# Kernel tuning notes

Measured on AMD Instinct MI355X. Metric: run time of the kernel, lower is better.

Reference implementation:

```python
import jax, jax.numpy as jnp
import numpy as np

N = 2048

def setup_inputs() -> dict:
    key = jax.random.key(0)
    ks = jax.random.split(key, 7)
    x = jax.random.uniform(ks[0], (N,), dtype=jnp.float32) * 100.0  # time vector
    W1 = jax.random.normal(ks[1], (128, 2), dtype=jnp.float32) * 0.5
    b1 = jax.random.normal(ks[2], (128,), dtype=jnp.float32) * 0.1
    W2 = jax.random.normal(ks[3], (32, 128), dtype=jnp.float32) * 0.1
    b2 = jax.random.normal(ks[4], (32,), dtype=jnp.float32) * 0.1
    W3 = jax.random.normal(ks[5], (1, 32), dtype=jnp.float32) * 0.1
    b3 = jax.random.normal(ks[6], (1,), dtype=jnp.float32) * 0.1
    return {"x": x, "W1": W1, "b1": b1, "W2": W2, "b2": b2, "W3": W3, "b3": b3}

def reference(x, W1, b1, W2, b2, W3, b3):
    # Vectorized equivalent of the nested-loop pair build:
    # pairs (x[i], x[j]) for all j >= i (upper triangle incl. diagonal).
    n = x.shape[0]
    iu_r, iu_c = np.triu_indices(n)  # static index arrays, P = n(n+1)/2
    pairs = jnp.stack([x[iu_r], x[iu_c]], axis=-1)  # [P, 2]
    h = jax.nn.sigmoid(pairs @ W1.T + b1)           # [P, 128]
    h = jax.nn.relu(h @ W2.T + b2)                  # [P, 32]
    v = (h @ W3.T + b3)[:, 0]                       # [P]
    # K starts as eye; the loops overwrite the full upper triangle (incl. diag),
    # leaving the strictly-lower triangle at 0.
    K = jnp.zeros((n, n), dtype=x.dtype).at[iu_r, iu_c].set(v)
    return K.T @ K  # torch casts to double; kept float32 (jax x64 disabled)
```

## Files before the change

kernel.cpp:

```cpp
#include <hip/hip_runtime.h>
#include <hip/hip_bf16.h>

#define N 2048

using f32x4  = __attribute__((ext_vector_type(4))) float;
using short8 = __attribute__((ext_vector_type(8))) short;
using uint4v = __attribute__((ext_vector_type(4))) unsigned int;

#define GLOAD_LDS16(dst, src)                                                        \
  __builtin_amdgcn_global_load_lds((const __attribute__((address_space(1))) void*)(src), \
                                   (__attribute__((address_space(3))) void*)(dst), 16, 0, 0)

__global__ void prep(const float* __restrict__ W2, const float* __restrict__ W1,
                     const float* __restrict__ b1,
                     __hip_bfloat16* __restrict__ W2b,
                     float* __restrict__ W1n, float* __restrict__ b1n) {
  const float c = -1.4426950408889634f;
  int t = blockIdx.x * 256 + threadIdx.x;
  W2b[t] = __float2bfloat16(W2[t]);
  if (t < 256) W1n[t] = W1[t] * c;
  if (t < 128) b1n[t] = b1[t] * c;
}

__global__ void zero_A(uint4v* __restrict__ A4) {
  A4[blockIdx.x * 256 + threadIdx.x] = (uint4v){0u, 0u, 0u, 0u};
}

__global__ __launch_bounds__(256) void build_A_mfma(
    const float* __restrict__ x,
    const float* __restrict__ W1n,
    const float* __restrict__ b1n,
    const __hip_bfloat16* __restrict__ W2b,
    const float* __restrict__ b2,
    const float* __restrict__ W3,
    const float* __restrict__ b3,
    __hip_bfloat16* __restrict__ A)
{
  const int t = blockIdx.x;
  int bj = (int)((sqrtf(8.0f * (float)t + 1.0f) - 1.0f) * 0.5f);
  while ((bj + 1) * (bj + 2) / 2 <= t) ++bj;
  while (bj * (bj + 1) / 2 > t) --bj;
  const int bi = t - bj * (bj + 1) / 2;

  const int i0 = bi * 16, j0 = bj * 16;
  const int tid = threadIdx.x;

  __shared__ float w1s[256];
  __shared__ float b1s[128];
  w1s[tid] = W1n[tid & 255];
  if (tid < 128) b1s[tid] = b1n[tid];
  __syncthreads();

  const int w  = tid >> 6;
  const int l  = tid & 63;
  const int lm = l & 15;
  const int lk = l >> 4;

  const float xi = x[i0 + lm];
  float xj[4];
#pragma unroll
  for (int m = 0; m < 4; ++m) xj[m] = x[j0 + w * 4 + m];

  short8 wf[2][4];
#pragma unroll
  for (int g = 0; g < 2; ++g)
#pragma unroll
    for (int kb = 0; kb < 4; ++kb)
      wf[g][kb] = *(const short8*)(W2b + (g * 16 + lm) * 128 + kb * 32 + lk * 8);

  const float b2v[2] = {b2[lm], b2[16 + lm]};
  f32x4 acc[4][2];
#pragma unroll
  for (int m = 0; m < 4; ++m)
#pragma unroll
    for (int g = 0; g < 2; ++g)
      acc[m][g] = (f32x4){b2v[g], b2v[g], b2v[g], b2v[g]};

#pragma unroll
  for (int kb = 0; kb < 4; ++kb) {
    float base[8], w1b_[8];
#pragma unroll
    for (int e = 0; e < 8; ++e) {
      const int k = kb * 32 + lk * 8 + e;
      base[e]  = fmaf(w1s[2 * k], xi, b1s[k]);
      w1b_[e]  = w1s[2 * k + 1];
    }
#pragma unroll
    for (int m = 0; m < 4; ++m) {
      uint4v pk;
#pragma unroll
      for (int e2 = 0; e2 < 4; ++e2) {
        const float t0 = fmaf(w1b_[2 * e2],     xj[m], base[2 * e2]);
        const float t1 = fmaf(w1b_[2 * e2 + 1], xj[m], base[2 * e2 + 1]);
        const float h0 = __builtin_amdgcn_rcpf(1.0f + __builtin_amdgcn_exp2f(t0));
        const float h1 = __builtin_amdgcn_rcpf(1.0f + __builtin_amdgcn_exp2f(t1));
        const unsigned u0 = __builtin_bit_cast(unsigned, h0) + 0x8000u;
        const unsigned u1 = __builtin_bit_cast(unsigned, h1) + 0x8000u;
        pk[e2] = __builtin_amdgcn_perm(u1, u0, 0x07060302u);
      }
      const short8 af = __builtin_bit_cast(short8, pk);
      acc[m][0] = __builtin_amdgcn_mfma_f32_16x16x32_bf16(af, wf[0][kb], acc[m][0], 0, 0, 0);
      acc[m][1] = __builtin_amdgcn_mfma_f32_16x16x32_bf16(af, wf[1][kb], acc[m][1], 0, 0, 0);
    }
  }

  const float w3a = W3[lm], w3b = W3[16 + lm];
  const float b3v = b3[0];
  const int   rsel = l & 3;

#pragma unroll
  for (int m = 0; m < 4; ++m) {
    const int j = j0 + w * 4 + m;
    float v[4];
#pragma unroll
    for (int r = 0; r < 4; ++r) {
      float s = fmaf(fmaxf(acc[m][0][r], 0.0f), w3a,
                     fmaxf(acc[m][1][r], 0.0f) * w3b);
      s += __shfl_xor(s, 1);
      s += __shfl_xor(s, 2);
      s += __shfl_xor(s, 4);
      s += __shfl_xor(s, 8);
      v[r] = s + b3v;
    }
    const float sv = rsel == 0 ? v[0] : rsel == 1 ? v[1] : rsel == 2 ? v[2] : v[3];
    const int i = i0 + lk * 4 + rsel;
    if (lm < 4 && i <= j)
      A[(size_t)j * N + i] = __float2bfloat16(sv);
  }
}

__global__ __launch_bounds__(256) void gemm_ata(
    const __hip_bfloat16* __restrict__ A, float* __restrict__ C)
{
  __shared__ __align__(16) __hip_bfloat16 As[64 * 32];
  __shared__ __align__(16) __hip_bfloat16 Bs[64 * 32];

  const int m0 = blockIdx.y * 64;
  const int n0 = blockIdx.x * 64;
  const int tid = threadIdx.x;
  const int w  = tid >> 6;
  const int l  = tid & 63;
  const int wr = (w >> 1) * 32;
  const int wc = (w & 1) * 32;
  const int lm = l & 15;
  const int lk = l >> 4;

  f32x4 acc[2][2];
#pragma unroll
  for (int m = 0; m < 2; ++m)
#pragma unroll
    for (int n = 0; n < 2; ++n)
      acc[m][n] = (f32x4){0.f, 0.f, 0.f, 0.f};

  const int mn = m0 < n0 ? m0 : n0;
  const int ktiles = (mn + 64) >> 5;

  const int srow = 16 * w + (l >> 2);
  const int scol = (l & 3) * 8;

  for (int kt = 0; kt < ktiles; ++kt) {
    const int k0 = kt * 32;
    __syncthreads();
    GLOAD_LDS16(As + 16 * w * 32, A + (size_t)(m0 + srow) * N + k0 + scol);
    GLOAD_LDS16(Bs + 16 * w * 32, A + (size_t)(n0 + srow) * N + k0 + scol);
    __syncthreads();

    short8 af[2], bfr[2];
#pragma unroll
    for (int m = 0; m < 2; ++m)
      af[m] = *(const short8*)(As + (wr + m * 16 + lm) * 32 + lk * 8);
#pragma unroll
    for (int n = 0; n < 2; ++n)
      bfr[n] = *(const short8*)(Bs + (wc + n * 16 + lm) * 32 + lk * 8);

#pragma unroll
    for (int m = 0; m < 2; ++m)
#pragma unroll
      for (int n = 0; n < 2; ++n)
        acc[m][n] = __builtin_amdgcn_mfma_f32_16x16x32_bf16(af[m], bfr[n], acc[m][n], 0, 0, 0);
  }

#pragma unroll
  for (int m = 0; m < 2; ++m) {
    const int row = m0 + wr + m * 16 + lk * 4;
#pragma unroll
    for (int n = 0; n < 2; ++n) {
      const int col = n0 + wc + n * 16 + lm;
#pragma unroll
      for (int r = 0; r < 4; ++r)
        C[(size_t)(row + r) * N + col] = acc[m][n][r];
    }
  }
}

extern "C" void kernel_launch(void* const* d_in, const int* in_sizes, int n_in,
                              void* d_out, int out_size, void* d_ws, size_t ws_size,
                              hipStream_t stream) {
  const float* x  = (const float*)d_in[0];
  const float* W1 = (const float*)d_in[1];
  const float* b1 = (const float*)d_in[2];
  const float* W2 = (const float*)d_in[3];
  const float* b2 = (const float*)d_in[4];
  const float* W3 = (const float*)d_in[5];
  const float* b3 = (const float*)d_in[6];
  float* C = (float*)d_out;

  __hip_bfloat16* W2b = (__hip_bfloat16*)d_ws;
  float* W1n = (float*)((char*)d_ws + 8192);
  float* b1n = (float*)((char*)d_ws + 12288);
  __hip_bfloat16* A = (__hip_bfloat16*)((char*)d_ws + 16384);

  prep<<<dim3(16), dim3(256), 0, stream>>>(W2, W1, b1, W2b, W1n, b1n);
  zero_A<<<dim3(2048), dim3(256), 0, stream>>>((uint4v*)A);
  build_A_mfma<<<dim3(8256), dim3(256), 0, stream>>>(x, W1n, b1n, W2b, b2, W3, b3, A);
  gemm_ata<<<dim3(32, 32), dim3(256), 0, stream>>>(A, C);
}
```

Before: 179.0 us.

## Fuse prep with zeroing, pack sigmoid math, enlarge and double-buffer GEMM tiles

Merges the weight-prep and A-zeroing kernels into one launch. Rewrites the first-layer pre-activation as two-wide float vectors so the compiler can emit packed FMA and add. Changes the A^T A GEMM from 64x64 to 128x128 block tiles with a 4x4 MFMA accumulator grid per wave and double-buffered LDS staging to overlap loads with compute. The larger tiles cut redundant global reads but launch only 256 blocks, and the triangular k-range gives those blocks uneven work.

```diff
diff --git a/kernel.cpp b/kernel.cpp
--- a/kernel.cpp
+++ b/kernel.cpp
@@ -3,6 +3,7 @@
 
 #define N 2048
 
+using f32x2  = __attribute__((ext_vector_type(2))) float;
 using f32x4  = __attribute__((ext_vector_type(4))) float;
 using short8 = __attribute__((ext_vector_type(8))) short;
 using uint4v = __attribute__((ext_vector_type(4))) unsigned int;
@@ -11,19 +12,17 @@
   __builtin_amdgcn_global_load_lds((const __attribute__((address_space(1))) void*)(src), \
                                    (__attribute__((address_space(3))) void*)(dst), 16, 0, 0)
 
-__global__ void prep(const float* __restrict__ W2, const float* __restrict__ W1,
-                     const float* __restrict__ b1,
-                     __hip_bfloat16* __restrict__ W2b,
-                     float* __restrict__ W1n, float* __restrict__ b1n) {
+__global__ void prep_zero(const float* __restrict__ W2, const float* __restrict__ W1,
+                          const float* __restrict__ b1,
+                          __hip_bfloat16* __restrict__ W2b,
+                          float* __restrict__ W1n, float* __restrict__ b1n,
+                          uint4v* __restrict__ A4) {
+  const int t = blockIdx.x * 256 + threadIdx.x;
+  A4[t] = (uint4v){0u, 0u, 0u, 0u};
   const float c = -1.4426950408889634f;
-  int t = blockIdx.x * 256 + threadIdx.x;
-  W2b[t] = __float2bfloat16(W2[t]);
-  if (t < 256) W1n[t] = W1[t] * c;
-  if (t < 128) b1n[t] = b1[t] * c;
-}
-
-__global__ void zero_A(uint4v* __restrict__ A4) {
-  A4[blockIdx.x * 256 + threadIdx.x] = (uint4v){0u, 0u, 0u, 0u};
+  if (t < 4096) W2b[t] = __float2bfloat16(W2[t]);
+  if (t < 256)  W1n[t] = W1[t] * c;
+  if (t < 128)  b1n[t] = b1[t] * c;
 }
 
 __global__ __launch_bounds__(256) void build_A_mfma(
@@ -78,22 +77,27 @@
 
 #pragma unroll
   for (int kb = 0; kb < 4; ++kb) {
-    float base[8], w1b_[8];
-#pragma unroll
-    for (int e = 0; e < 8; ++e) {
-      const int k = kb * 32 + lk * 8 + e;
-      base[e]  = fmaf(w1s[2 * k], xi, b1s[k]);
-      w1b_[e]  = w1s[2 * k + 1];
+    f32x2 basep[4], w1bp[4];
+#pragma unroll
+    for (int e2 = 0; e2 < 4; ++e2) {
+      const int k = kb * 32 + lk * 8 + e2 * 2;
+      basep[e2] = (f32x2){fmaf(w1s[2 * k],     xi, b1s[k]),
+                          fmaf(w1s[2 * k + 2], xi, b1s[k + 1])};
+      w1bp[e2]  = (f32x2){w1s[2 * k + 1], w1s[2 * k + 3]};
     }
 #pragma unroll
     for (int m = 0; m < 4; ++m) {
+      const f32x2 xj2 = (f32x2){xj[m], xj[m]};
       uint4v pk;
 #pragma unroll
       for (int e2 = 0; e2 < 4; ++e2) {
-        const float t0 = fmaf(w1b_[2 * e2],     xj[m], base[2 * e2]);
-        const float t1 = fmaf(w1b_[2 * e2 + 1], xj[m], base[2 * e2 + 1]);
-        const float h0 = __builtin_amdgcn_rcpf(1.0f + __builtin_amdgcn_exp2f(t0));
-        const float h1 = __builtin_amdgcn_rcpf(1.0f + __builtin_amdgcn_exp2f(t1));
+        const f32x2 t01 = __builtin_elementwise_fma(w1bp[e2], xj2, basep[e2]);
+        f32x2 e01;
+        e01[0] = __builtin_amdgcn_exp2f(t01[0]);
+        e01[1] = __builtin_amdgcn_exp2f(t01[1]);
+        const f32x2 d01 = e01 + (f32x2){1.0f, 1.0f};
+        const float h0 = __builtin_amdgcn_rcpf(d01[0]);
+        const float h1 = __builtin_amdgcn_rcpf(d01[1]);
         const unsigned u0 = __builtin_bit_cast(unsigned, h0) + 0x8000u;
         const unsigned u1 = __builtin_bit_cast(unsigned, h1) + 0x8000u;
         pk[e2] = __builtin_amdgcn_perm(u1, u0, 0x07060302u);
@@ -132,59 +136,74 @@
 __global__ __launch_bounds__(256) void gemm_ata(
     const __hip_bfloat16* __restrict__ A, float* __restrict__ C)
 {
-  __shared__ __align__(16) __hip_bfloat16 As[64 * 32];
-  __shared__ __align__(16) __hip_bfloat16 Bs[64 * 32];
-
-  const int m0 = blockIdx.y * 64;
-  const int n0 = blockIdx.x * 64;
+  __shared__ __align__(16) __hip_bfloat16 As[2][128 * 32];
+  __shared__ __align__(16) __hip_bfloat16 Bs[2][128 * 32];
+
+  const int m0 = blockIdx.y * 128;
+  const int n0 = blockIdx.x * 128;
   const int tid = threadIdx.x;
   const int w  = tid >> 6;
   const int l  = tid & 63;
-  const int wr = (w >> 1) * 32;
-  const int wc = (w & 1) * 32;
+  const int wr = (w >> 1) * 64;
+  const int wc = (w & 1) * 64;
   const int lm = l & 15;
   const int lk = l >> 4;
 
-  f32x4 acc[2][2];
-#pragma unroll
-  for (int m = 0; m < 2; ++m)
-#pragma unroll
-    for (int n = 0; n < 2; ++n)
+  f32x4 acc[4][4];
+#pragma unroll
+  for (int m = 0; m < 4; ++m)
+#pragma unroll
+    for (int n = 0; n < 4; ++n)
       acc[m][n] = (f32x4){0.f, 0.f, 0.f, 0.f};
 
   const int mn = m0 < n0 ? m0 : n0;
-  const int ktiles = (mn + 64) >> 5;
-
-  const int srow = 16 * w + (l >> 2);
+  const int ktiles = (mn + 128) >> 5;
+
+  const int srow = l >> 2;
   const int scol = (l & 3) * 8;
 
+#define STAGE(kt, b)                                                                   \
+  {                                                                                    \
+    const int k0_ = (kt) * 32;                                                         \
+    _Pragma("unroll")                                                                  \
+    for (int c = 0; c < 2; ++c) {                                                      \
+      const int r0 = (w * 2 + c) * 16;                                                 \
+      GLOAD_LDS16(&As[b][r0 * 32], A + (size_t)(m0 + r0 + srow) * N + k0_ + scol);     \
+      GLOAD_LDS16(&Bs[b][r0 * 32], A + (size_t)(n0 + r0 + srow) * N + k0_ + scol);     \
+    }                                                                                  \
+  }
+
+  STAGE(0, 0);
+  __syncthreads();
+
   for (int kt = 0; kt < ktiles; ++kt) {
-    const int k0 = kt * 32;
+    const int cur = kt & 1;
+    if (kt + 1 < ktiles)
+      STAGE(kt + 1, cur ^ 1);
+
+    short8 af[4], bfr[4];
+#pragma unroll
+    for (int m = 0; m < 4; ++m)
+      af[m] = *(const short8*)(&As[cur][(wr + m * 16 + lm) * 32 + lk * 8]);
+#pragma unroll
+    for (int n = 0; n < 4; ++n)
+      bfr[n] = *(const short8*)(&Bs[cur][(wc + n * 16 + lm) * 32 + lk * 8]);
+
+#pragma unroll
+    for (int m = 0; m < 4; ++m)
+#pragma unroll
+      for (int n = 0; n < 4; ++n)
+        acc[m][n] = __builtin_amdgcn_mfma_f32_16x16x32_bf16(af[m], bfr[n], acc[m][n], 0, 0, 0);
+
     __syncthreads();
-    GLOAD_LDS16(As + 16 * w * 32, A + (size_t)(m0 + srow) * N + k0 + scol);
-    GLOAD_LDS16(Bs + 16 * w * 32, A + (size_t)(n0 + srow) * N + k0 + scol);
-    __syncthreads();
-
-    short8 af[2], bfr[2];
-#pragma unroll
-    for (int m = 0; m < 2; ++m)
-      af[m] = *(const short8*)(As + (wr + m * 16 + lm) * 32 + lk * 8);
-#pragma unroll
-    for (int n = 0; n < 2; ++n)
-      bfr[n] = *(const short8*)(Bs + (wc + n * 16 + lm) * 32 + lk * 8);
-
-#pragma unroll
-    for (int m = 0; m < 2; ++m)
-#pragma unroll
-      for (int n = 0; n < 2; ++n)
-        acc[m][n] = __builtin_amdgcn_mfma_f32_16x16x32_bf16(af[m], bfr[n], acc[m][n], 0, 0, 0);
-  }
-
-#pragma unroll
-  for (int m = 0; m < 2; ++m) {
+  }
+#undef STAGE
+
+#pragma unroll
+  for (int m = 0; m < 4; ++m) {
     const int row = m0 + wr + m * 16 + lk * 4;
 #pragma unroll
-    for (int n = 0; n < 2; ++n) {
+    for (int n = 0; n < 4; ++n) {
       const int col = n0 + wc + n * 16 + lm;
 #pragma unroll
       for (int r = 0; r < 4; ++r)
@@ -210,8 +229,7 @@
   float* b1n = (float*)((char*)d_ws + 12288);
   __hip_bfloat16* A = (__hip_bfloat16*)((char*)d_ws + 16384);
 
-  prep<<<dim3(16), dim3(256), 0, stream>>>(W2, W1, b1, W2b, W1n, b1n);
-  zero_A<<<dim3(2048), dim3(256), 0, stream>>>((uint4v*)A);
+  prep_zero<<<dim3(2048), dim3(256), 0, stream>>>(W2, W1, b1, W2b, W1n, b1n, (uint4v*)A);
   build_A_mfma<<<dim3(8256), dim3(256), 0, stream>>>(x, W1n, b1n, W2b, b2, W3, b3, A);
-  gemm_ata<<<dim3(32, 32), dim3(256), 0, stream>>>(A, C);
-}
+  gemm_ata<<<dim3(16, 16), dim3(256), 0, stream>>>(A, C);
+}
```

Result: slower. 183.1 us (+2.3%).
